# Optimization experiments

Hardware: AMD Instinct MI355X
Metric: run time of the kernel (lower is better)

The kernel has to match this reference:

```python
import jax, jax.numpy as jnp
import numpy as np

D = 1024
B, N = 4, 2048

def setup_inputs() -> dict:
    key = jax.random.key(0)
    ks = jax.random.split(key, 7)
    sc = 1.0 / np.sqrt(D)
    return {
        "x": jax.random.normal(ks[0], (B, N, D), dtype=jnp.float32),
        "wq_w": jax.random.normal(ks[1], (D, D), dtype=jnp.float32) * sc,
        "wq_b": jax.random.normal(ks[2], (D,), dtype=jnp.float32) * 0.01,
        "wk_w": jax.random.normal(ks[3], (D, D), dtype=jnp.float32) * sc,
        "wk_b": jax.random.normal(ks[4], (D,), dtype=jnp.float32) * 0.01,
        "wv_w": jax.random.normal(ks[5], (D, D), dtype=jnp.float32) * sc,
        "wv_b": jax.random.normal(ks[6], (D,), dtype=jnp.float32) * 0.01,
    }

def reference(x, wq_w, wq_b, wk_w, wk_b, wv_w, wv_b):
    # torch Linear: y = x @ W^T + b
    q = x @ wq_w.T + wq_b
    k = x @ wk_w.T + wk_b
    v = x @ wv_w.T + wv_b
    d = q.shape[-1]
    s = jnp.einsum("bid,bjd->bij", q, k) / jnp.sqrt(jnp.float32(d))
    # faithful to original: triu then transpose (zeros, NOT -inf, enter the softmax)
    t = jnp.swapaxes(jnp.triu(s), -2, -1)
    p = jax.nn.softmax(t, axis=-2)
    attn = jnp.swapaxes(jnp.triu(p), -2, -1) @ v
    return attn
```

## Files before the change

### kernel.cpp

```cpp
#include <hip/hip_runtime.h>
#include <hip/hip_fp16.h>
#include <cstdint>

typedef _Float16 half8_t __attribute__((ext_vector_type(8)));
typedef float f32x4 __attribute__((ext_vector_type(4)));

#define D_ 1024
#define B_ 4
#define N_ 2048
#define M_ (B_*N_)
#define NC_ 3072

#define OFF_WCAT  0u
#define OFF_BCAT  6291456u
#define OFF_XB    6303744u
#define OFF_Q     23080960u
#define OFF_K     39858176u
#define OFF_V     56635392u
#define OFF_ZP    73412608u
#define OFF_DEXP  74461184u
#define OFF_SV    74493952u

__device__ __forceinline__ void gload_lds16(const void* g, void* l) {
  __builtin_amdgcn_global_load_lds(
      (const __attribute__((address_space(1))) unsigned int*)(uintptr_t)g,
      (__attribute__((address_space(3))) unsigned int*)(uintptr_t)l, 16, 0, 0);
}

__device__ __forceinline__ void stage128x64(const __half* rowbase, char* lds, int tid) {
#pragma unroll
  for (int inst = 0; inst < 4; ++inst) {
    int L  = inst * 4096 + tid * 16;
    int r  = L >> 7;
    int cb = L & 127;
    int cbs = cb ^ ((r & 7) << 4);
    gload_lds16((const char*)rowbase + (size_t)r * (D_ * 2) + cbs, lds + L);
  }
}

__device__ __forceinline__ half8_t ldsfrag(const char* lds, int row, int cbyte) {
  int b = (row << 7) + (cbyte ^ ((row & 7) << 4));
  return *reinterpret_cast<const half8_t*>(lds + b);
}

__device__ __forceinline__ void gemm128_core(const __half* Arow0, const __half* Brow0,
                                             char* As, char* Bs, f32x4 acc[4][4]) {
  const int tid  = threadIdx.x;
  const int lane = tid & 63;
  const int wave = tid >> 6;
  const int wm = wave >> 1, wn = wave & 1;
  for (int kt = 0; kt < 16; ++kt) {
    if (kt) __syncthreads();
    stage128x64(Arow0 + kt * 64, As, tid);
    stage128x64(Brow0 + kt * 64, Bs, tid);
    asm volatile("s_waitcnt vmcnt(0)" ::: "memory");
    __syncthreads();
#pragma unroll
    for (int kk = 0; kk < 2; ++kk) {
      const int cbyte = kk * 64 + (lane >> 4) * 16;
      half8_t a[4], b[4];
#pragma unroll
      for (int mf = 0; mf < 4; ++mf) a[mf] = ldsfrag(As, wm * 64 + mf * 16 + (lane & 15), cbyte);
#pragma unroll
      for (int nf = 0; nf < 4; ++nf) b[nf] = ldsfrag(Bs, wn * 64 + nf * 16 + (lane & 15), cbyte);
#pragma unroll
      for (int mf = 0; mf < 4; ++mf)
#pragma unroll
        for (int nf = 0; nf < 4; ++nf)
          acc[mf][nf] = __builtin_amdgcn_mfma_f32_16x16x32_f16(a[mf], b[nf], acc[mf][nf], 0, 0, 0);
    }
  }
}

__device__ __forceinline__ void calc_soff(int tid, int soff[4]) {
#pragma unroll
  for (int i = 0; i < 4; ++i) {
    int L = i * 8192 + tid * 16;
    int s = L >> 10;
    int w = L & 1023;
    w ^= ((w >> 9) & 1) << 5;
    int r  = (s >> 1) * 16 + (w >> 6);
    int kb = (s & 1) * 64 + (w & 63);
    soff[i] = r * 2048 + kb;
  }
}

#define MFMA_QUAD(QM, QN)                                                     \
  _Pragma("unroll")                                                           \
  for (int ks = 0; ks < 2; ++ks)                                              \
    _Pragma("unroll")                                                         \
    for (int mf = 0; mf < 4; ++mf)                                            \
      _Pragma("unroll")                                                       \
      for (int nf = 0; nf < 2; ++nf)                                          \
        acc[(QM)*4 + mf][(QN)*2 + nf] = __builtin_amdgcn_mfma_f32_16x16x32_f16( \
            a[mf][ks], b[(QN)][nf][ks], acc[(QM)*4 + mf][(QN)*2 + nf], 0, 0, 0);

__device__ __forceinline__ void gemm256_8ph(const char* Ag, const char* Bg,
                                            char* smem, f32x4 acc[8][4]) {
  const int tid  = threadIdx.x;
  const int lane = tid & 63;
  const int wave = tid >> 6;
  const int wm = wave >> 2, wn = wave & 3;

  int soff[4];
  calc_soff(tid, soff);
  const int wlane = (((lane & 15) * 64 + (lane >> 4) * 16)) ^ (((lane >> 3) & 1) << 5);

#pragma unroll
  for (int i = 0; i < 4; ++i) gload_lds16(Ag + soff[i], smem + i * 8192 + tid * 16);
#pragma unroll
  for (int i = 0; i < 4; ++i) gload_lds16(Bg + soff[i], smem + 32768 + i * 8192 + tid * 16);
  asm volatile("s_waitcnt vmcnt(0)" ::: "memory");
  __builtin_amdgcn_s_barrier();

  for (int t = 0; t < 16; ++t) {
    char* A0  = smem + ((t & 1) << 16);
    char* B0  = A0 + 32768;
    char* A1  = smem + (((t + 1) & 1) << 16);
    char* B1s = A1 + 32768;
    const half8_t* ap = (const half8_t*)(A0 + wm * 16384 + wlane);
    const half8_t* bp = (const half8_t*)(B0 + wn * 8192 + wlane);
    const char* Agn = Ag + (t + 1) * 128;
    const char* Bgn = Bg + (t + 1) * 128;
    const bool pre = (t < 15);

    half8_t a[4][2];
    half8_t b[2][2][2];

#pragma unroll
    for (int mf = 0; mf < 4; ++mf)
#pragma unroll
      for (int ks = 0; ks < 2; ++ks)
        a[mf][ks] = ap[(mf * 2 + ks) * 64];
#pragma unroll
    for (int nf = 0; nf < 2; ++nf)
#pragma unroll
      for (int ks = 0; ks < 2; ++ks)
        b[0][nf][ks] = bp[(nf * 2 + ks) * 64];
    if (pre) {
#pragma unroll
      for (int i = 0; i < 4; ++i) gload_lds16(Agn + soff[i], A1 + i * 8192 + tid * 16);
    }
    __builtin_amdgcn_s_barrier();
    asm volatile("s_waitcnt lgkmcnt(0)" ::: "memory");
    __builtin_amdgcn_s_setprio(1);
    MFMA_QUAD(0, 0)
    __builtin_amdgcn_s_setprio(0);
    __builtin_amdgcn_s_barrier();

#pragma unroll
    for (int nf = 0; nf < 2; ++nf)
#pragma unroll
      for (int ks = 0; ks < 2; ++ks)
        b[1][nf][ks] = bp[((2 + nf) * 2 + ks) * 64];
    if (pre) {
#pragma unroll
      for (int i = 0; i < 4; ++i) gload_lds16(Bgn + soff[i], B1s + i * 8192 + tid * 16);
    }
    __builtin_amdgcn_s_barrier();
    asm volatile("s_waitcnt lgkmcnt(0)" ::: "memory");
    __builtin_amdgcn_s_setprio(1);
    MFMA_QUAD(0, 1)
    __builtin_amdgcn_s_setprio(0);
    __builtin_amdgcn_s_barrier();

#pragma unroll
    for (int mf = 0; mf < 4; ++mf)
#pragma unroll
      for (int ks = 0; ks < 2; ++ks)
        a[mf][ks] = ap[((4 + mf) * 2 + ks) * 64];
    __builtin_amdgcn_s_barrier();
    asm volatile("s_waitcnt lgkmcnt(0)" ::: "memory");
    __builtin_amdgcn_s_setprio(1);
    MFMA_QUAD(1, 0)
    __builtin_amdgcn_s_setprio(0);
    __builtin_amdgcn_s_barrier();

    __builtin_amdgcn_s_setprio(1);
    MFMA_QUAD(1, 1)
    __builtin_amdgcn_s_setprio(0);
    if (pre) asm volatile("s_waitcnt vmcnt(0)" ::: "memory");
    __builtin_amdgcn_s_barrier();
  }
}

__global__ __launch_bounds__(256) void k_prep(
    const float* __restrict__ x, const float* __restrict__ wq, const float* __restrict__ wk,
    const float* __restrict__ wv, const float* __restrict__ bq, const float* __restrict__ bk,
    const float* __restrict__ bv, __half* __restrict__ xb, __half* __restrict__ wcat,
    float* __restrict__ bcat) {
  const int NX4 = (M_ * D_) / 4;
  const int NW4 = (D_ * D_) / 4;
  const int TOT = NX4 + 3 * NW4;
  int tid0 = blockIdx.x * 256 + threadIdx.x;
  int stride = gridDim.x * 256;
  for (int i = tid0; i < TOT; i += stride) {
    float4 f; __half* dst;
    if (i < NX4) {
      f = ((const float4*)x)[i];
      dst = xb + 4 * (size_t)i;
    } else {
      int j = i - NX4; int w = j / NW4; int o = j - w * NW4;
      const float* src = (w == 0) ? wq : (w == 1) ? wk : wv;
      f = ((const float4*)src)[o];
      dst = wcat + (size_t)w * (D_ * D_) + 4 * (size_t)o;
    }
    __half h0 = __float2half(f.x), h1 = __float2half(f.y),
           h2 = __float2half(f.z), h3 = __float2half(f.w);
    ushort4 u = { __half_as_ushort(h0), __half_as_ushort(h1),
                  __half_as_ushort(h2), __half_as_ushort(h3) };
    *((ushort4*)dst) = u;
  }
  if (tid0 < NC_)
    bcat[tid0] = (tid0 < 1024) ? bq[tid0] : (tid0 < 2048) ? bk[tid0 - 1024] : bv[tid0 - 2048];
}

__global__ __launch_bounds__(256) void k_qkv(
    const __half* __restrict__ xb, const __half* __restrict__ wcat,
    const float* __restrict__ bcat,
    __half* __restrict__ q, __half* __restrict__ kx, __half* __restrict__ v) {
  __shared__ __align__(16) char smem[32768];
  char* As = smem; char* Bs = smem + 16384;
  int bid = blockIdx.x;
  int bm = bid / 24, bn = bid % 24;
  f32x4 acc[4][4];
#pragma unroll
  for (int i = 0; i < 4; ++i)
#pragma unroll
    for (int j = 0; j < 4; ++j) acc[i][j] = f32x4{0.f, 0.f, 0.f, 0.f};
  gemm128_core(xb + (size_t)bm * 128 * D_, wcat + (size_t)bn * 128 * D_, As, Bs, acc);

  const int lane = threadIdx.x & 63;
  const int wave = threadIdx.x >> 6;
  const int wm = wave >> 1, wn = wave & 1;
  int sel = bn >> 3;
  __half* outp = (sel == 0) ? q : (sel == 1) ? kx : v;
#pragma unroll
  for (int nf = 0; nf < 4; ++nf) {
    int nloc = wn * 64 + nf * 16 + (lane & 15);
    float bias = bcat[bn * 128 + nloc];
    int ncol = (bn & 7) * 128 + nloc;
#pragma unroll
    for (int mf = 0; mf < 4; ++mf) {
#pragma unroll
      for (int r = 0; r < 4; ++r) {
        int m = bm * 128 + wm * 64 + mf * 16 + (lane >> 4) * 4 + r;
        outp[(size_t)m * D_ + ncol] = __float2half(acc[mf][nf][r] + bias);
      }
    }
  }
}

__global__ __launch_bounds__(512, 2) void k_stats256(
    const __half* __restrict__ q, const __half* __restrict__ kx,
    const __half* __restrict__ v,
    float* __restrict__ Zpart, float* __restrict__ dexp, float* __restrict__ Sv) {
  __shared__ __align__(16) char smem[131072];
  int bid = blockIdx.x;
  int tile = (bid & 7) * 22 + (bid >> 3);

  if (tile >= 144) {
    int sid = tile - 144;
    int half = threadIdx.x >> 8;
    int dg = threadIdx.x & 255;
    int d0 = dg * 4;
#pragma unroll
    for (int it = 0; it < 4; ++it) {
      int slab = sid * 8 + half * 4 + it;
      int b = slab >> 6, c = slab & 63;
      const ushort4* vp = (const ushort4*)(v + ((size_t)(b * N_ + c * 32)) * D_ + d0);
      f32x4 s = {0.f, 0.f, 0.f, 0.f};
#pragma unroll 8
      for (int r2 = 0; r2 < 32; ++r2) {
        ushort4 u = vp[r2 * (D_ / 4)];
        s[0] += __half2float(__ushort_as_half(u.x));
        s[1] += __half2float(__ushort_as_half(u.y));
        s[2] += __half2float(__ushort_as_half(u.z));
        s[3] += __half2float(__ushort_as_half(u.w));
      }
      *(f32x4*)(Sv + (size_t)slab * D_ + d0) = s;
    }
    return;
  }

  int b = tile / 36;
  int r = tile % 36;
  int ti = 0;
  while (r >= 8 - ti) { r -= 8 - ti; ++ti; }
  int tj = ti + r;

  f32x4 acc[8][4];
#pragma unroll
  for (int i = 0; i < 8; ++i)
#pragma unroll
    for (int j = 0; j < 4; ++j) acc[i][j] = f32x4{0.f, 0.f, 0.f, 0.f};

  const size_t base = (size_t)b * N_ * D_;
  gemm256_8ph((const char*)(q + base + (size_t)ti * 256 * D_),
              (const char*)(kx + base + (size_t)tj * 256 * D_), smem, acc);

  const int lane = threadIdx.x & 63;
  const int wave = threadIdx.x >> 6;
  const int wm = wave >> 2, wn = wave & 3;
  const bool offd = (tj > ti);
  const float scale = 0.03125f;
  int zr0 = b * N_ + ti * 256;
#pragma unroll
  for (int mf = 0; mf < 8; ++mf) {
#pragma unroll
    for (int rr = 0; rr < 4; ++rr) {
      int il = wm * 128 + mf * 16 + (lane >> 4) * 4 + rr;
      float ssum = 0.f;
#pragma unroll
      for (int nf = 0; nf < 4; ++nf) {
        int jl = wn * 64 + nf * 16 + (lane & 15);
        float e = __expf(acc[mf][nf][rr] * scale);
        bool keep = offd || (jl >= il);
        if (!offd && jl == il) dexp[zr0 + il] = e;
        ssum += keep ? e : 0.f;
      }
      ssum += __shfl_xor(ssum, 1);
      ssum += __shfl_xor(ssum, 2);
      ssum += __shfl_xor(ssum, 4);
      ssum += __shfl_xor(ssum, 8);
      if ((lane & 15) == 0)
        Zpart[(size_t)(zr0 + il) * 32 + tj * 4 + wn] = ssum;
    }
  }
}

__global__ __launch_bounds__(256) void k_out(
    const __half* __restrict__ v, const float* __restrict__ Sv,
    const float* __restrict__ Zpart, const float* __restrict__ dexp,
    float* __restrict__ out) {
  __shared__ float sInv[32], sCd[32];
  int slab = blockIdx.x;
  int b = slab >> 6, c = slab & 63;
  int dg = threadIdx.x;
  int d0 = dg * 4;
  int zi0 = b * N_ + c * 32;

  if (dg < 32) {
    int i  = c * 32 + dg;
    int row = zi0 + dg;
    int t0 = (i >> 8) * 4;
    float z = 0.f;
    for (int t = t0; t < 32; ++t) z += Zpart[(size_t)row * 32 + t];
    float iv = 1.f / ((float)i + z);
    sInv[dg] = iv;
    sCd[dg]  = dexp[row] * iv;
  }
  __syncthreads();

  f32x4 run = {0.f, 0.f, 0.f, 0.f};
  for (int cc = 0; cc < c; ++cc) {
    f32x4 sv = *(const f32x4*)(Sv + (size_t)((b << 6) + cc) * D_ + d0);
    run[0] += sv[0]; run[1] += sv[1]; run[2] += sv[2]; run[3] += sv[3];
  }
  const ushort4* vp = (const ushort4*)(v + (size_t)zi0 * D_ + d0);
  float* op = out + (size_t)zi0 * D_ + d0;
#pragma unroll 4
  for (int r2 = 0; r2 < 32; ++r2) {
    ushort4 u = vp[r2 * (D_ / 4)];
    f32x4 vi;
    vi[0] = __half2float(__ushort_as_half(u.x));
    vi[1] = __half2float(__ushort_as_half(u.y));
    vi[2] = __half2float(__ushort_as_half(u.z));
    vi[3] = __half2float(__ushort_as_half(u.w));
    float iv = sInv[r2], cd = sCd[r2];
    f32x4 o;
    o[0] = run[0] * iv + cd * vi[0];
    o[1] = run[1] * iv + cd * vi[1];
    o[2] = run[2] * iv + cd * vi[2];
    o[3] = run[3] * iv + cd * vi[3];
    *(f32x4*)(op + (size_t)r2 * D_) = o;
    run[0] += vi[0]; run[1] += vi[1]; run[2] += vi[2]; run[3] += vi[3];
  }
}

extern "C" void kernel_launch(void* const* d_in, const int* in_sizes, int n_in,
                              void* d_out, int out_size, void* d_ws, size_t ws_size,
                              hipStream_t stream) {
  const float* x  = (const float*)d_in[0];
  const float* wq = (const float*)d_in[1];
  const float* bq = (const float*)d_in[2];
  const float* wk = (const float*)d_in[3];
  const float* bk = (const float*)d_in[4];
  const float* wv = (const float*)d_in[5];
  const float* bv = (const float*)d_in[6];
  float* out = (float*)d_out;
  char* ws = (char*)d_ws;

  __half* wcat = (__half*)(ws + OFF_WCAT);
  float*  bcat = (float*)(ws + OFF_BCAT);
  __half* xb   = (__half*)(ws + OFF_XB);
  __half* q    = (__half*)(ws + OFF_Q);
  __half* k    = (__half*)(ws + OFF_K);
  __half* v    = (__half*)(ws + OFF_V);
  float* Zpart = (float*)(ws + OFF_ZP);
  float* dexp  = (float*)(ws + OFF_DEXP);
  float* Sv    = (float*)(ws + OFF_SV);

  k_prep<<<dim3(2048), dim3(256), 0, stream>>>(x, wq, wk, wv, bq, bk, bv, xb, wcat, bcat);
  k_qkv<<<dim3(64 * 24), dim3(256), 0, stream>>>(xb, wcat, bcat, q, k, v);
  k_stats256<<<dim3(176), dim3(512), 0, stream>>>(q, k, v, Zpart, dexp, Sv);
  k_out<<<dim3(256), dim3(256), 0, stream>>>(v, Sv, Zpart, dexp, out);
}
```

Before: 133.8 us.

## Replace QKV GEMM with 256x192 double-buffered, software-pipelined MFMA kernel

Replaces the 128x128-tile QKV projection GEMM, which was single-buffered and synchronous, with a 256x192-tile kernel that uses 512 threads and 8 waves. Even and odd K-slices are double-buffered in LDS, and the global-to-LDS prefetch of the next slices is interleaved with MFMA phases using fine-grained barriers, vmcnt waits and s_setprio. Blocks are remapped across XCDs. The aim is to hide memory latency and raise arithmetic intensity, at the cost of 112KB of LDS per block, one block per CU, and a wave of 512 tiles that may not evenly fill the CUs.

```diff
diff --git a/kernel.cpp b/kernel.cpp
--- a/kernel.cpp
+++ b/kernel.cpp
@@ -25,51 +25,6 @@
   __builtin_amdgcn_global_load_lds(
       (const __attribute__((address_space(1))) unsigned int*)(uintptr_t)g,
       (__attribute__((address_space(3))) unsigned int*)(uintptr_t)l, 16, 0, 0);
-}
-
-__device__ __forceinline__ void stage128x64(const __half* rowbase, char* lds, int tid) {
-#pragma unroll
-  for (int inst = 0; inst < 4; ++inst) {
-    int L  = inst * 4096 + tid * 16;
-    int r  = L >> 7;
-    int cb = L & 127;
-    int cbs = cb ^ ((r & 7) << 4);
-    gload_lds16((const char*)rowbase + (size_t)r * (D_ * 2) + cbs, lds + L);
-  }
-}
-
-__device__ __forceinline__ half8_t ldsfrag(const char* lds, int row, int cbyte) {
-  int b = (row << 7) + (cbyte ^ ((row & 7) << 4));
-  return *reinterpret_cast<const half8_t*>(lds + b);
-}
-
-__device__ __forceinline__ void gemm128_core(const __half* Arow0, const __half* Brow0,
-                                             char* As, char* Bs, f32x4 acc[4][4]) {
-  const int tid  = threadIdx.x;
-  const int lane = tid & 63;
-  const int wave = tid >> 6;
-  const int wm = wave >> 1, wn = wave & 1;
-  for (int kt = 0; kt < 16; ++kt) {
-    if (kt) __syncthreads();
-    stage128x64(Arow0 + kt * 64, As, tid);
-    stage128x64(Brow0 + kt * 64, Bs, tid);
-    asm volatile("s_waitcnt vmcnt(0)" ::: "memory");
-    __syncthreads();
-#pragma unroll
-    for (int kk = 0; kk < 2; ++kk) {
-      const int cbyte = kk * 64 + (lane >> 4) * 16;
-      half8_t a[4], b[4];
-#pragma unroll
-      for (int mf = 0; mf < 4; ++mf) a[mf] = ldsfrag(As, wm * 64 + mf * 16 + (lane & 15), cbyte);
-#pragma unroll
-      for (int nf = 0; nf < 4; ++nf) b[nf] = ldsfrag(Bs, wn * 64 + nf * 16 + (lane & 15), cbyte);
-#pragma unroll
-      for (int mf = 0; mf < 4; ++mf)
-#pragma unroll
-        for (int nf = 0; nf < 4; ++nf)
-          acc[mf][nf] = __builtin_amdgcn_mfma_f32_16x16x32_f16(a[mf], b[nf], acc[mf][nf], 0, 0, 0);
-    }
-  }
 }
 
 __device__ __forceinline__ void calc_soff(int tid, int soff[4]) {
@@ -215,37 +170,179 @@
     bcat[tid0] = (tid0 < 1024) ? bq[tid0] : (tid0 < 2048) ? bk[tid0 - 1024] : bv[tid0 - 2048];
 }
 
-__global__ __launch_bounds__(256) void k_qkv(
+#define QG01(QM)                                                             \
+  _Pragma("unroll") for (int ks = 0; ks < 2; ++ks)                           \
+  _Pragma("unroll") for (int mf = 0; mf < 4; ++mf)                           \
+  _Pragma("unroll") for (int nf = 0; nf < 2; ++nf)                           \
+    acc[(QM)*4+mf][nf] = __builtin_amdgcn_mfma_f32_16x16x32_f16(             \
+        a[mf][ks], b[nf][ks], acc[(QM)*4+mf][nf], 0, 0, 0);
+
+#define QG2(QM)                                                              \
+  _Pragma("unroll") for (int ks = 0; ks < 2; ++ks)                           \
+  _Pragma("unroll") for (int mf = 0; mf < 4; ++mf)                           \
+    acc[(QM)*4+mf][2] = __builtin_amdgcn_mfma_f32_16x16x32_f16(              \
+        a[mf][ks], b[2][ks], acc[(QM)*4+mf][2], 0, 0, 0);
+
+#define STGA(DST, SRC, I) gload_lds16((SRC) + soffA[I], (DST) + (I) * 8192 + tid * 16);
+#define STGB(DST, SRC, I) gload_lds16((SRC) + soffB[I], (DST) + (I) * 8192 + tid * 16);
+
+__global__ __launch_bounds__(512, 1) void k_qkv192(
     const __half* __restrict__ xb, const __half* __restrict__ wcat,
     const float* __restrict__ bcat,
     __half* __restrict__ q, __half* __restrict__ kx, __half* __restrict__ v) {
-  __shared__ __align__(16) char smem[32768];
-  char* As = smem; char* Bs = smem + 16384;
+  __shared__ __align__(16) char smem[114688];
+  const int tid  = threadIdx.x;
+  const int lane = tid & 63;
+  const int wave = tid >> 6;
+  const int wm = wave >> 2, wn = wave & 3;
+
   int bid = blockIdx.x;
-  int bm = bid / 24, bn = bid % 24;
-  f32x4 acc[4][4];
-#pragma unroll
-  for (int i = 0; i < 4; ++i)
-#pragma unroll
-    for (int j = 0; j < 4; ++j) acc[i][j] = f32x4{0.f, 0.f, 0.f, 0.f};
-  gemm128_core(xb + (size_t)bm * 128 * D_, wcat + (size_t)bn * 128 * D_, As, Bs, acc);
-
-  const int lane = threadIdx.x & 63;
-  const int wave = threadIdx.x >> 6;
-  const int wm = wave >> 1, wn = wave & 1;
-  int sel = bn >> 3;
-  __half* outp = (sel == 0) ? q : (sel == 1) ? kx : v;
-#pragma unroll
-  for (int nf = 0; nf < 4; ++nf) {
-    int nloc = wn * 64 + nf * 16 + (lane & 15);
-    float bias = bcat[bn * 128 + nloc];
-    int ncol = (bn & 7) * 128 + nloc;
-#pragma unroll
-    for (int mf = 0; mf < 4; ++mf) {
-#pragma unroll
-      for (int r = 0; r < 4; ++r) {
-        int m = bm * 128 + wm * 64 + mf * 16 + (lane >> 4) * 4 + r;
-        outp[(size_t)m * D_ + ncol] = __float2half(acc[mf][nf][r] + bias);
+  int wgid = (bid & 7) * 64 + (bid >> 3);
+  int bm = wgid >> 4, bn = wgid & 15;
+
+  float bias[3];
+#pragma unroll
+  for (int nf = 0; nf < 3; ++nf)
+    bias[nf] = bcat[bn * 192 + wn * 48 + nf * 16 + (lane & 15)];
+  asm volatile("" :: "v"(bias[0]), "v"(bias[1]), "v"(bias[2]));
+
+  int soffA[4], soffB[3];
+#pragma unroll
+  for (int i = 0; i < 4; ++i) {
+    int L = i * 8192 + tid * 16;
+    int s = L >> 10, w = L & 1023;
+    w ^= ((w >> 9) & 1) << 5;
+    soffA[i] = ((s >> 1) * 16 + (w >> 6)) * 2048 + ((s & 1) * 64 + (w & 63));
+  }
+#pragma unroll
+  for (int i = 0; i < 3; ++i) {
+    int L = i * 8192 + tid * 16;
+    int s = L >> 10, w = L & 1023;
+    w ^= ((w >> 9) & 1) << 5;
+    soffB[i] = ((s >> 1) * 16 + (w >> 6)) * 2048 + ((s & 1) * 64 + (w & 63));
+  }
+  const int wlane = (((lane & 15) * 64 + (lane >> 4) * 16)) ^ (((lane >> 3) & 1) << 5);
+
+  const char* Ag = (const char*)(xb + (size_t)bm * 256 * D_);
+  const char* Bg = (const char*)(wcat + (size_t)bn * 192 * D_);
+  char* Ae = smem;           char* Be = smem + 32768;
+  char* Ao = smem + 57344;   char* Bo = smem + 90112;
+
+  f32x4 acc[8][3];
+#pragma unroll
+  for (int i = 0; i < 8; ++i)
+#pragma unroll
+    for (int j = 0; j < 3; ++j) acc[i][j] = f32x4{0.f, 0.f, 0.f, 0.f};
+
+#pragma unroll
+  for (int i = 0; i < 4; ++i) STGA(Ae, Ag, i)
+#pragma unroll
+  for (int i = 0; i < 3; ++i) STGB(Be, Bg, i)
+#pragma unroll
+  for (int i = 0; i < 4; ++i) STGA(Ao, Ag + 128, i)
+#pragma unroll
+  for (int i = 0; i < 3; ++i) STGB(Bo, Bg + 128, i)
+  asm volatile("s_waitcnt vmcnt(7)" ::: "memory");
+  __builtin_amdgcn_s_barrier();
+
+  half8_t a[4][2], b[3][2];
+  for (int it = 0; it < 8; ++it) {
+    const bool pre = (it < 7);
+    const char* Ag2 = Ag + (2 * it + 2) * 128;
+    const char* Bg2 = Bg + (2 * it + 2) * 128;
+    const char* Ag3 = Ag + (2 * it + 3) * 128;
+    const char* Bg3 = Bg + (2 * it + 3) * 128;
+    const half8_t* apE = (const half8_t*)(Ae + wm * 16384 + wlane);
+    const half8_t* bpE = (const half8_t*)(Be + wn * 6144  + wlane);
+    const half8_t* apO = (const half8_t*)(Ao + wm * 16384 + wlane);
+    const half8_t* bpO = (const half8_t*)(Bo + wn * 6144  + wlane);
+
+#pragma unroll
+    for (int mf = 0; mf < 4; ++mf)
+#pragma unroll
+      for (int ks = 0; ks < 2; ++ks) a[mf][ks] = apE[(mf * 2 + ks) * 64];
+#pragma unroll
+    for (int nf = 0; nf < 2; ++nf)
+#pragma unroll
+      for (int ks = 0; ks < 2; ++ks) b[nf][ks] = bpE[(nf * 2 + ks) * 64];
+    __builtin_amdgcn_s_barrier();
+    asm volatile("s_waitcnt lgkmcnt(0)" ::: "memory");
+    __builtin_amdgcn_s_setprio(1); QG01(0) __builtin_amdgcn_s_setprio(0);
+    __builtin_amdgcn_s_barrier();
+
+#pragma unroll
+    for (int ks = 0; ks < 2; ++ks) b[2][ks] = bpE[(4 + ks) * 64];
+    __builtin_amdgcn_s_barrier();
+    asm volatile("s_waitcnt lgkmcnt(0)" ::: "memory");
+    __builtin_amdgcn_s_setprio(1); QG2(0) __builtin_amdgcn_s_setprio(0);
+    __builtin_amdgcn_s_barrier();
+
+#pragma unroll
+    for (int mf = 0; mf < 4; ++mf)
+#pragma unroll
+      for (int ks = 0; ks < 2; ++ks) a[mf][ks] = apE[((4 + mf) * 2 + ks) * 64];
+    if (pre) { STGB(Be, Bg2, 0) STGB(Be, Bg2, 1) }
+    __builtin_amdgcn_s_barrier();
+    asm volatile("s_waitcnt lgkmcnt(0)" ::: "memory");
+    __builtin_amdgcn_s_setprio(1); QG01(1) __builtin_amdgcn_s_setprio(0);
+    __builtin_amdgcn_s_barrier();
+
+    if (pre) { STGB(Be, Bg2, 2) STGA(Ae, Ag2, 0) }
+    __builtin_amdgcn_s_setprio(1); QG2(1) __builtin_amdgcn_s_setprio(0);
+    if (pre) asm volatile("s_waitcnt vmcnt(4)" ::: "memory");
+    else     asm volatile("s_waitcnt vmcnt(0)" ::: "memory");
+    __builtin_amdgcn_s_barrier();
+
+#pragma unroll
+    for (int mf = 0; mf < 4; ++mf)
+#pragma unroll
+      for (int ks = 0; ks < 2; ++ks) a[mf][ks] = apO[(mf * 2 + ks) * 64];
+#pragma unroll
+    for (int nf = 0; nf < 2; ++nf)
+#pragma unroll
+      for (int ks = 0; ks < 2; ++ks) b[nf][ks] = bpO[(nf * 2 + ks) * 64];
+    if (pre) { STGA(Ae, Ag2, 1) STGA(Ae, Ag2, 2) }
+    __builtin_amdgcn_s_barrier();
+    asm volatile("s_waitcnt lgkmcnt(0)" ::: "memory");
+    __builtin_amdgcn_s_setprio(1); QG01(0) __builtin_amdgcn_s_setprio(0);
+    __builtin_amdgcn_s_barrier();
+
+#pragma unroll
+    for (int ks = 0; ks < 2; ++ks) b[2][ks] = bpO[(4 + ks) * 64];
+    if (pre) { STGA(Ae, Ag2, 3) }
+    __builtin_amdgcn_s_barrier();
+    asm volatile("s_waitcnt lgkmcnt(0)" ::: "memory");
+    __builtin_amdgcn_s_setprio(1); QG2(0) __builtin_amdgcn_s_setprio(0);
+    __builtin_amdgcn_s_barrier();
+
+#pragma unroll
+    for (int mf = 0; mf < 4; ++mf)
+#pragma unroll
+      for (int ks = 0; ks < 2; ++ks) a[mf][ks] = apO[((4 + mf) * 2 + ks) * 64];
+    if (pre) { STGB(Bo, Bg3, 0) STGB(Bo, Bg3, 1) }
+    __builtin_amdgcn_s_barrier();
+    asm volatile("s_waitcnt lgkmcnt(0)" ::: "memory");
+    __builtin_amdgcn_s_setprio(1); QG01(1) __builtin_amdgcn_s_setprio(0);
+    __builtin_amdgcn_s_barrier();
+
+    if (pre) { STGB(Bo, Bg3, 2) STGA(Ao, Ag3, 0) STGA(Ao, Ag3, 1)
+               STGA(Ao, Ag3, 2) STGA(Ao, Ag3, 3) }
+    __builtin_amdgcn_s_setprio(1); QG2(1) __builtin_amdgcn_s_setprio(0);
+    if (pre) asm volatile("s_waitcnt vmcnt(7)" ::: "memory");
+    __builtin_amdgcn_s_barrier();
+  }
+
+#pragma unroll
+  for (int nf = 0; nf < 3; ++nf) {
+    int gcol = bn * 192 + wn * 48 + nf * 16 + (lane & 15);
+    int sel = gcol >> 10, col = gcol & 1023;
+    __half* outp = (sel == 0) ? q : (sel == 1) ? kx : v;
+#pragma unroll
+    for (int mf = 0; mf < 8; ++mf) {
+#pragma unroll
+      for (int rr = 0; rr < 4; ++rr) {
+        int m = bm * 256 + wm * 128 + mf * 16 + (lane >> 4) * 4 + rr;
+        outp[(size_t)m * D_ + col] = __float2half(acc[mf][nf][rr] + bias[nf]);
       }
     }
   }
@@ -402,7 +499,7 @@
   float* Sv    = (float*)(ws + OFF_SV);
 
   k_prep<<<dim3(2048), dim3(256), 0, stream>>>(x, wq, wk, wv, bq, bk, bv, xb, wcat, bcat);
-  k_qkv<<<dim3(64 * 24), dim3(256), 0, stream>>>(xb, wcat, bcat, q, k, v);
+  k_qkv192<<<dim3(512), dim3(512), 0, stream>>>(xb, wcat, bcat, q, k, v);
   k_stats256<<<dim3(176), dim3(512), 0, stream>>>(q, k, v, Zpart, dexp, Sv);
   k_out<<<dim3(256), dim3(256), 0, stream>>>(v, Sv, Zpart, dexp, out);
 }
```

After: 132.1 us. Within noise of the previous version (-1.3%).
